# Performance work log

Measured on AMD Instinct MI355X. Metric: run time of the kernel, lower is better.

## Reference

```python
import jax, jax.numpy as jnp
import numpy as np

N, R, B, H, C, E = 4096, 8, 30, 64, 16, 131072


def setup_inputs() -> dict:
    key = jax.random.key(0)
    ks = jax.random.split(key, 11)
    s = 0.02  # small init scale for weights
    return {
        "x": jax.random.normal(ks[0], (N, N), jnp.float32),
        "edge_index": jax.random.randint(ks[1], (2, E), 0, N, jnp.int32),
        "edge_type": jax.random.randint(ks[2], (E,), 0, R, jnp.int32),
        "basis1": jax.random.normal(ks[3], (B, N, H), jnp.float32) * s,
        "att1": jax.random.normal(ks[4], (R, B), jnp.float32) * s,
        "root1": jax.random.normal(ks[5], (N, H), jnp.float32) * s,
        "bias1": jnp.zeros((H,), jnp.float32),
        "basis2": jax.random.normal(ks[6], (B, H, C), jnp.float32) * s,
        "att2": jax.random.normal(ks[7], (R, B), jnp.float32) * s,
        "root2": jax.random.normal(ks[8], (H, C), jnp.float32) * s,
        "bias2": jnp.zeros((C,), jnp.float32),
    }


def _rgcn_conv(x, src, dst, etype, deg_inv, basis, att, root, bias):
    # Basis-decomposed relation weights: W_r = sum_b att[r,b] * basis[b]
    W = jnp.einsum("rb,bio->rio", att, basis)            # [R, in, out]
    # Pre-transform every node by every relation weight (equivalent to
    # per-edge bmm(x_j, W[edge_type]) but avoids gathering [E, in] features).
    h = jnp.einsum("ni,rio->nro", x, W)                  # [N, R, out]
    msg = h[src, etype]                                  # [E, out] per-edge message
    agg = jax.ops.segment_sum(msg, dst, num_segments=N)  # scatter-add to dst
    agg = agg * deg_inv[:, None]                         # scatter-mean (aggr='mean')
    return agg + x @ root + bias                         # root/self transform + bias


def reference(x, edge_index, edge_type, basis1, att1, root1, bias1,
              basis2, att2, root2, bias2):
    src, dst = edge_index[0], edge_index[1]
    deg = jax.ops.segment_sum(jnp.ones((E,), jnp.float32), dst, num_segments=N)
    deg_inv = 1.0 / jnp.maximum(deg, 1.0)  # zero in-degree -> 0 output, as scatter_mean
    h = jax.nn.relu(_rgcn_conv(x, src, dst, edge_type, deg_inv,
                               basis1, att1, root1, bias1))
    out = _rgcn_conv(h, src, dst, edge_type, deg_inv,
                     basis2, att2, root2, bias2)
    return jax.nn.log_softmax(out, axis=1)
```

## Files before the change

kernel.cpp:

```cpp
#include <hip/hip_runtime.h>
#include <cstdint>

#define E_CNT 131072
#define N_CNT 4096

typedef short bf16x8 __attribute__((ext_vector_type(8)));
typedef float f32x4 __attribute__((ext_vector_type(4)));

__device__ __forceinline__ ushort f2bf(float f) {
  union { float f; unsigned u; } v; v.f = f;
  unsigned r = v.u + 0x7FFFu + ((v.u >> 16) & 1u);
  return (ushort)(r >> 16);
}

__global__ __launch_bounds__(256) void k_combine(const float* __restrict__ att1,
                                                 const float* __restrict__ basis1,
                                                 const float* __restrict__ root1,
                                                 ushort* __restrict__ wt1,
                                                 const int* __restrict__ dstp,
                                                 int* __restrict__ deg) {
  __shared__ float sT[32 * 33];
  int bid = blockIdx.x, t = threadIdx.x;
  if (bid < 256) {
    int i0 = (bid >> 1) * 32, o0 = (bid & 1) * 32;
    int ol = t & 31, ir = t >> 5;
    float a[8][4] = {};
    for (int b = 0; b < 30; b += 2) {
      float v0[4], v1[4];
#pragma unroll
      for (int k = 0; k < 4; ++k) {
        size_t ofs = (size_t)(i0 + ir + k * 8) * 64 + o0 + ol;
        v0[k] = basis1[(size_t)b * 262144 + ofs];
        v1[k] = basis1[(size_t)(b + 1) * 262144 + ofs];
      }
#pragma unroll
      for (int r = 0; r < 8; ++r) {
        float w0 = att1[r * 30 + b], w1 = att1[r * 30 + b + 1];
#pragma unroll
        for (int k = 0; k < 4; ++k) a[r][k] += w0 * v0[k] + w1 * v1[k];
      }
    }
    for (int r = 0; r < 8; ++r) {
#pragma unroll
      for (int k = 0; k < 4; ++k) sT[ol * 33 + ir + k * 8] = a[r][k];
      __syncthreads();
#pragma unroll
      for (int k = 0; k < 4; ++k) {
        int orow = ir + k * 8, icol = ol;
        wt1[(size_t)(r * 64 + o0 + orow) * 4096 + i0 + icol] = f2bf(sT[orow * 33 + icol]);
      }
      __syncthreads();
    }
  } else if (bid < 384) {
    int bb = bid - 256;
    int i0 = bb * 32;
    int ol = t & 31, ir = t >> 5;
    for (int oh = 0; oh < 2; ++oh) {
      int o0 = oh * 32;
#pragma unroll
      for (int k = 0; k < 4; ++k)
        sT[ol * 33 + ir + k * 8] = root1[(size_t)(i0 + ir + k * 8) * 64 + o0 + ol];
      __syncthreads();
#pragma unroll
      for (int k = 0; k < 4; ++k) {
        int orow = ir + k * 8, icol = ol;
        wt1[(size_t)(512 + o0 + orow) * 4096 + i0 + icol] = f2bf(sT[orow * 33 + icol]);
      }
      __syncthreads();
    }
  } else {
    int e = (bid - 384) * 256 + t;
    atomicAdd(&deg[dstp[e]], 1);
  }
}

__global__ __launch_bounds__(1024) void k_scan(const int* __restrict__ deg,
                                               int* __restrict__ rowptr,
                                               int* __restrict__ cursor,
                                               float* __restrict__ dinv) {
  __shared__ int part[1024];
  int t = threadIdx.x;
  int base = t * 4;
  int d0 = deg[base], d1 = deg[base + 1], d2 = deg[base + 2], d3 = deg[base + 3];
  int s = d0 + d1 + d2 + d3;
  part[t] = s;
  __syncthreads();
  for (int off = 1; off < 1024; off <<= 1) {
    int v = part[t];
    int u = (t >= off) ? part[t - off] : 0;
    __syncthreads();
    part[t] = v + u;
    __syncthreads();
  }
  int incl = part[t];
  int excl = incl - s;
  int p0 = excl, p1 = excl + d0, p2 = p1 + d1, p3 = p2 + d2;
  rowptr[base] = p0; rowptr[base + 1] = p1; rowptr[base + 2] = p2; rowptr[base + 3] = p3;
  cursor[base] = p0; cursor[base + 1] = p1; cursor[base + 2] = p2; cursor[base + 3] = p3;
  dinv[base]     = 1.0f / fmaxf((float)d0, 1.0f);
  dinv[base + 1] = 1.0f / fmaxf((float)d1, 1.0f);
  dinv[base + 2] = 1.0f / fmaxf((float)d2, 1.0f);
  dinv[base + 3] = 1.0f / fmaxf((float)d3, 1.0f);
  if (t == 1023) rowptr[4096] = incl;
}

__global__ __launch_bounds__(256) void k_mid(const int* __restrict__ srcp,
                                             const int* __restrict__ dstp,
                                             const int* __restrict__ et,
                                             int* __restrict__ cursor,
                                             int* __restrict__ spack,
                                             const float* __restrict__ att2,
                                             const float* __restrict__ basis2,
                                             const float* __restrict__ root2,
                                             float* __restrict__ w2e) {
  int bid = blockIdx.x, t = threadIdx.x;
  if (bid < 512) {
    int e = bid * 256 + t;
    int d = dstp[e];
    int pos = atomicAdd(&cursor[d], 1);
    spack[pos] = (srcp[e] << 3) | et[e];
  } else {
    int r = bid - 512;
    for (int q = t; q < 1024; q += 256) {
      float a = 0.f;
      if (r < 8) {
        for (int b = 0; b < 30; ++b) a += att2[r * 30 + b] * basis2[b * 1024 + q];
      } else {
        a = root2[q];
      }
      w2e[r * 1024 + q] = a;
    }
  }
}

__global__ __launch_bounds__(256, 5) void k_gemm1(const float* __restrict__ x,
                                                  const ushort* __restrict__ wt1,
                                                  float* __restrict__ c1) {
  __shared__ __align__(16) ushort As[128 * 64];
  __shared__ __align__(16) ushort Bs[64 * 64];
  int bid = blockIdx.x;
  int xcd = bid & 7, idx = bid >> 3;
  int bn = idx % 9, mk = idx / 9;
  int kp = xcd >> 1, bm = ((xcd & 1) << 4) + mk;
  int m0 = bm * 128, n0 = bn * 64, kbase = kp * 1024;
  int tid = threadIdx.x;
  int lane = tid & 63, wid = tid >> 6;
  int wm = wid >> 1, wn = wid & 1;

  f32x4 acc[4][2] = {};

  for (int tt = 0; tt < 16; ++tt) {
    int k0 = kbase + tt * 64;
    float4 va[4][2];
#pragma unroll
    for (int it = 0; it < 4; ++it) {
      int flat = it * 256 + tid;
      int row = flat >> 3, gg = flat & 7;
      const float* src = x + (size_t)(m0 + row) * 4096 + k0 + ((gg ^ (row & 7)) << 3);
      va[it][0] = *(const float4*)src;
      va[it][1] = *(const float4*)(src + 4);
    }
#pragma unroll
    for (int it = 0; it < 2; ++it) {
      int flat = it * 256 + tid;
      int row = flat >> 3, gg = flat & 7;
      int gcol = k0 + ((gg ^ (row & 7)) << 3);
      const ushort* g = wt1 + (size_t)(n0 + row) * 4096 + gcol;
      ushort* l = &Bs[(it * 256 + wid * 64) * 8];
      __builtin_amdgcn_global_load_lds((const __attribute__((address_space(1))) void*)g,
                                       (__attribute__((address_space(3))) void*)l, 16, 0, 0);
    }
#pragma unroll
    for (int it = 0; it < 4; ++it) {
      int flat = it * 256 + tid;
      float4 v0 = va[it][0], v1 = va[it][1];
      ushort o8[8] = {f2bf(v0.x), f2bf(v0.y), f2bf(v0.z), f2bf(v0.w),
                      f2bf(v1.x), f2bf(v1.y), f2bf(v1.z), f2bf(v1.w)};
      *(ulonglong2*)&As[flat * 8] = *(const ulonglong2*)o8;
    }
    __syncthreads();
    int q = lane >> 4, sw = lane & 7, r16 = lane & 15;
#pragma unroll
    for (int ks = 0; ks < 2; ++ks) {
      int co = ((ks * 4 + q) ^ sw) << 3;
      bf16x8 b0 = *(const bf16x8*)&Bs[(wn * 32 + 0 * 16 + r16) * 64 + co];
      bf16x8 b1 = *(const bf16x8*)&Bs[(wn * 32 + 1 * 16 + r16) * 64 + co];
      bf16x8 a0 = *(const bf16x8*)&As[(wm * 64 + 0 * 16 + r16) * 64 + co];
      bf16x8 a1 = *(const bf16x8*)&As[(wm * 64 + 1 * 16 + r16) * 64 + co];
      bf16x8 a2 = *(const bf16x8*)&As[(wm * 64 + 2 * 16 + r16) * 64 + co];
      bf16x8 a3 = *(const bf16x8*)&As[(wm * 64 + 3 * 16 + r16) * 64 + co];
      __builtin_amdgcn_s_setprio(1);
      acc[0][0] = __builtin_amdgcn_mfma_f32_16x16x32_bf16(a0, b0, acc[0][0], 0, 0, 0);
      acc[0][1] = __builtin_amdgcn_mfma_f32_16x16x32_bf16(a0, b1, acc[0][1], 0, 0, 0);
      acc[1][0] = __builtin_amdgcn_mfma_f32_16x16x32_bf16(a1, b0, acc[1][0], 0, 0, 0);
      acc[1][1] = __builtin_amdgcn_mfma_f32_16x16x32_bf16(a1, b1, acc[1][1], 0, 0, 0);
      acc[2][0] = __builtin_amdgcn_mfma_f32_16x16x32_bf16(a2, b0, acc[2][0], 0, 0, 0);
      acc[2][1] = __builtin_amdgcn_mfma_f32_16x16x32_bf16(a2, b1, acc[2][1], 0, 0, 0);
      acc[3][0] = __builtin_amdgcn_mfma_f32_16x16x32_bf16(a3, b0, acc[3][0], 0, 0, 0);
      acc[3][1] = __builtin_amdgcn_mfma_f32_16x16x32_bf16(a3, b1, acc[3][1], 0, 0, 0);
      __builtin_amdgcn_s_setprio(0);
    }
    __syncthreads();
  }

  int cf = lane & 15, rf4 = (lane >> 4) * 4;
#pragma unroll
  for (int mi = 0; mi < 4; ++mi)
#pragma unroll
    for (int ni = 0; ni < 2; ++ni) {
      int gcol = n0 + wn * 32 + ni * 16 + cf;
#pragma unroll
      for (int j = 0; j < 4; ++j) {
        int grow = m0 + wm * 64 + mi * 16 + rf4 + j;
        atomicAdd(&c1[(size_t)grow * 576 + gcol], acc[mi][ni][j]);
      }
    }
}

__global__ __launch_bounds__(256) void k_agg1h2(const float* __restrict__ c1,
                                                const int* __restrict__ rowptr,
                                                const int* __restrict__ spack,
                                                const float* __restrict__ dinv,
                                                const float* __restrict__ bias1,
                                                const float* __restrict__ w2e,
                                                float* __restrict__ h2c) {
  __shared__ float sh[4][64];
  int g = threadIdx.x >> 6, t = threadIdx.x & 63;
  int n = blockIdx.x * 4 + g;
  int s0 = rowptr[n], s1 = rowptr[n + 1];
  float acc = 0.f;
  int e = s0;
  for (; e + 3 < s1; e += 4) {
    int p0 = spack[e], p1 = spack[e + 1], p2 = spack[e + 2], p3 = spack[e + 3];
    float v0 = c1[(size_t)(p0 >> 3) * 576 + (p0 & 7) * 64 + t];
    float v1 = c1[(size_t)(p1 >> 3) * 576 + (p1 & 7) * 64 + t];
    float v2 = c1[(size_t)(p2 >> 3) * 576 + (p2 & 7) * 64 + t];
    float v3 = c1[(size_t)(p3 >> 3) * 576 + (p3 & 7) * 64 + t];
    acc += (v0 + v1) + (v2 + v3);
  }
  for (; e < s1; ++e) {
    int p = spack[e];
    acc += c1[(size_t)(p >> 3) * 576 + (p & 7) * 64 + t];
  }
  float v = acc * dinv[n] + c1[(size_t)n * 576 + 512 + t] + bias1[t];
  sh[g][t] = fmaxf(v, 0.f);
  __syncthreads();
  float* o = h2c + (size_t)n * 144;
  for (int rc = t; rc < 144; rc += 64) {
    int r9 = rc >> 4, c = rc & 15;
    const float* w = w2e + r9 * 1024 + c;
    float a = 0.f;
#pragma unroll
    for (int hh = 0; hh < 64; ++hh) a += sh[g][hh] * w[hh * 16];
    o[rc] = a;
  }
}

__global__ __launch_bounds__(64) void k_agg2(const float* __restrict__ h2c,
                                             const int* __restrict__ rowptr,
                                             const int* __restrict__ spack,
                                             const float* __restrict__ dinv,
                                             const float* __restrict__ bias2,
                                             float* __restrict__ out) {
  __shared__ float red[64];
  int n = blockIdx.x, t = threadIdx.x;
  int c = t & 15, q = t >> 4;
  int s0 = rowptr[n], s1 = rowptr[n + 1];
  float acc = 0.f;
  for (int e = s0 + q; e < s1; e += 4) {
    int p = spack[e];
    acc += h2c[(size_t)(p >> 3) * 144 + (p & 7) * 16 + c];
  }
  red[t] = acc;
  __syncthreads();
  if (t < 16) {
    float sum = red[c] + red[16 + c] + red[32 + c] + red[48 + c];
    float v = sum * dinv[n] + h2c[(size_t)n * 144 + 128 + c] + bias2[c];
    float m = v;
#pragma unroll
    for (int off = 1; off < 16; off <<= 1) m = fmaxf(m, __shfl_xor(m, off, 64));
    float ex = expf(v - m);
    float s = ex;
#pragma unroll
    for (int off = 1; off < 16; off <<= 1) s += __shfl_xor(s, off, 64);
    out[n * 16 + c] = v - m - logf(s);
  }
}

extern "C" void kernel_launch(void* const* d_in, const int* in_sizes, int n_in,
                              void* d_out, int out_size, void* d_ws, size_t ws_size,
                              hipStream_t stream) {
  const float* x      = (const float*)d_in[0];
  const int*   ei     = (const int*)d_in[1];
  const int*   et     = (const int*)d_in[2];
  const float* basis1 = (const float*)d_in[3];
  const float* att1   = (const float*)d_in[4];
  const float* root1  = (const float*)d_in[5];
  const float* bias1  = (const float*)d_in[6];
  const float* basis2 = (const float*)d_in[7];
  const float* att2   = (const float*)d_in[8];
  const float* root2  = (const float*)d_in[9];
  const float* bias2  = (const float*)d_in[10];
  float* out = (float*)d_out;

  char* ws = (char*)d_ws;
  size_t off = 0;
  auto alloc = [&](size_t bytes) {
    void* p = ws + off;
    off = (off + bytes + 255) & ~(size_t)255;
    return p;
  };
  ushort* wt1  = (ushort*)alloc((size_t)576 * 4096 * 2);
  float*  c1   = (float*)alloc((size_t)N_CNT * 576 * 4);
  float*  w2e  = (float*)alloc((size_t)9 * 64 * 16 * 4);
  float*  h2c  = (float*)alloc((size_t)N_CNT * 144 * 4);
  int*    deg    = (int*)alloc(4096 * 4);
  float*  dinv   = (float*)alloc(4096 * 4);
  int*    rowptr = (int*)alloc(4097 * 4);
  int*    cursor = (int*)alloc(4096 * 4);
  int*    spack  = (int*)alloc((size_t)E_CNT * 4);

  const int* srcp = ei;
  const int* dstp = ei + E_CNT;

  hipMemsetAsync(deg, 0, 4096 * 4, stream);
  hipMemsetAsync(c1, 0, (size_t)N_CNT * 576 * 4, stream);
  k_combine<<<896, 256, 0, stream>>>(att1, basis1, root1, wt1, dstp, deg);
  k_scan<<<1, 1024, 0, stream>>>(deg, rowptr, cursor, dinv);
  k_mid<<<521, 256, 0, stream>>>(srcp, dstp, et, cursor, spack,
                                 att2, basis2, root2, w2e);
  k_gemm1<<<1152, 256, 0, stream>>>(x, wt1, c1);
  k_agg1h2<<<1024, 256, 0, stream>>>(c1, rowptr, spack, dinv, bias1, w2e, h2c);
  k_agg2<<<4096, 64, 0, stream>>>(h2c, rowptr, spack, dinv, bias2, out);
}
```

Measured before the change: 139.7 us.

## Pre-convert x to bf16 in prep kernel and stream GEMM tiles via direct LDS loads

Adds 8192 blocks to the prep kernel that convert the fp32 x matrix to a bf16 workspace copy. The GEMM then loads A tiles with global_load_lds like the B tiles, doubles the K tile to 128, and remaps the block swizzle. This takes the fp32 load and per-thread conversion out of the GEMM inner loop and halves A-operand bytes. In exchange it adds a full extra pass over x (64MB read plus 32MB write) and doubles LDS use, which lowers occupancy.

```diff
diff --git a/kernel.cpp b/kernel.cpp
--- a/kernel.cpp
+++ b/kernel.cpp
@@ -13,12 +13,14 @@
   return (ushort)(r >> 16);
 }
 
-__global__ __launch_bounds__(256) void k_combine(const float* __restrict__ att1,
-                                                 const float* __restrict__ basis1,
-                                                 const float* __restrict__ root1,
-                                                 ushort* __restrict__ wt1,
-                                                 const int* __restrict__ dstp,
-                                                 int* __restrict__ deg) {
+__global__ __launch_bounds__(256) void k_prep(const float* __restrict__ att1,
+                                              const float* __restrict__ basis1,
+                                              const float* __restrict__ root1,
+                                              ushort* __restrict__ wt1,
+                                              const int* __restrict__ dstp,
+                                              int* __restrict__ deg,
+                                              const float4* __restrict__ x,
+                                              ushort* __restrict__ xbf) {
   __shared__ float sT[32 * 33];
   int bid = blockIdx.x, t = threadIdx.x;
   if (bid < 256) {
@@ -68,9 +70,16 @@
       }
       __syncthreads();
     }
-  } else {
+  } else if (bid < 896) {
     int e = (bid - 384) * 256 + t;
     atomicAdd(&deg[dstp[e]], 1);
+  } else {
+    int i = (bid - 896) * 256 + t;
+    float4 v0 = x[i * 2], v1 = x[i * 2 + 1];
+    ushort o[8];
+    o[0] = f2bf(v0.x); o[1] = f2bf(v0.y); o[2] = f2bf(v0.z); o[3] = f2bf(v0.w);
+    o[4] = f2bf(v1.x); o[5] = f2bf(v1.y); o[6] = f2bf(v1.z); o[7] = f2bf(v1.w);
+    *(ulonglong2*)(xbf + (size_t)i * 8) = *(const ulonglong2*)o;
   }
 }
 
@@ -133,15 +142,15 @@
   }
 }
 
-__global__ __launch_bounds__(256, 5) void k_gemm1(const float* __restrict__ x,
+__global__ __launch_bounds__(256, 3) void k_gemm1(const ushort* __restrict__ xbf,
                                                   const ushort* __restrict__ wt1,
                                                   float* __restrict__ c1) {
-  __shared__ __align__(16) ushort As[128 * 64];
-  __shared__ __align__(16) ushort Bs[64 * 64];
+  __shared__ __align__(16) ushort As[128 * 128];
+  __shared__ __align__(16) ushort Bs[64 * 128];
   int bid = blockIdx.x;
-  int xcd = bid & 7, idx = bid >> 3;
-  int bn = idx % 9, mk = idx / 9;
-  int kp = xcd >> 1, bm = ((xcd & 1) << 4) + mk;
+  int swz = (bid & 7) * 144 + (bid >> 3);
+  int kp = swz / 288, rem = swz % 288;
+  int bm = rem / 9, bn = rem % 9;
   int m0 = bm * 128, n0 = bn * 64, kbase = kp * 1024;
   int tid = threadIdx.x;
   int lane = tid & 63, wid = tid >> 6;
@@ -149,46 +158,39 @@
 
   f32x4 acc[4][2] = {};
 
-  for (int tt = 0; tt < 16; ++tt) {
-    int k0 = kbase + tt * 64;
-    float4 va[4][2];
+  for (int tt = 0; tt < 8; ++tt) {
+    int k0 = kbase + tt * 128;
+#pragma unroll
+    for (int it = 0; it < 8; ++it) {
+      int flat = it * 256 + tid;
+      int row = flat >> 4, gg = flat & 15;
+      int gcol = k0 + ((gg ^ (row & 7)) << 3);
+      const ushort* g = xbf + (size_t)(m0 + row) * 4096 + gcol;
+      ushort* l = &As[(it * 256 + wid * 64) * 8];
+      __builtin_amdgcn_global_load_lds((const __attribute__((address_space(1))) void*)g,
+                                       (__attribute__((address_space(3))) void*)l, 16, 0, 0);
+    }
 #pragma unroll
     for (int it = 0; it < 4; ++it) {
       int flat = it * 256 + tid;
-      int row = flat >> 3, gg = flat & 7;
-      const float* src = x + (size_t)(m0 + row) * 4096 + k0 + ((gg ^ (row & 7)) << 3);
-      va[it][0] = *(const float4*)src;
-      va[it][1] = *(const float4*)(src + 4);
-    }
-#pragma unroll
-    for (int it = 0; it < 2; ++it) {
-      int flat = it * 256 + tid;
-      int row = flat >> 3, gg = flat & 7;
+      int row = flat >> 4, gg = flat & 15;
       int gcol = k0 + ((gg ^ (row & 7)) << 3);
       const ushort* g = wt1 + (size_t)(n0 + row) * 4096 + gcol;
       ushort* l = &Bs[(it * 256 + wid * 64) * 8];
       __builtin_amdgcn_global_load_lds((const __attribute__((address_space(1))) void*)g,
                                        (__attribute__((address_space(3))) void*)l, 16, 0, 0);
     }
-#pragma unroll
-    for (int it = 0; it < 4; ++it) {
-      int flat = it * 256 + tid;
-      float4 v0 = va[it][0], v1 = va[it][1];
-      ushort o8[8] = {f2bf(v0.x), f2bf(v0.y), f2bf(v0.z), f2bf(v0.w),
-                      f2bf(v1.x), f2bf(v1.y), f2bf(v1.z), f2bf(v1.w)};
-      *(ulonglong2*)&As[flat * 8] = *(const ulonglong2*)o8;
-    }
     __syncthreads();
     int q = lane >> 4, sw = lane & 7, r16 = lane & 15;
 #pragma unroll
-    for (int ks = 0; ks < 2; ++ks) {
+    for (int ks = 0; ks < 4; ++ks) {
       int co = ((ks * 4 + q) ^ sw) << 3;
-      bf16x8 b0 = *(const bf16x8*)&Bs[(wn * 32 + 0 * 16 + r16) * 64 + co];
-      bf16x8 b1 = *(const bf16x8*)&Bs[(wn * 32 + 1 * 16 + r16) * 64 + co];
-      bf16x8 a0 = *(const bf16x8*)&As[(wm * 64 + 0 * 16 + r16) * 64 + co];
-      bf16x8 a1 = *(const bf16x8*)&As[(wm * 64 + 1 * 16 + r16) * 64 + co];
-      bf16x8 a2 = *(const bf16x8*)&As[(wm * 64 + 2 * 16 + r16) * 64 + co];
-      bf16x8 a3 = *(const bf16x8*)&As[(wm * 64 + 3 * 16 + r16) * 64 + co];
+      bf16x8 b0 = *(const bf16x8*)&Bs[(wn * 32 + 0 * 16 + r16) * 128 + co];
+      bf16x8 b1 = *(const bf16x8*)&Bs[(wn * 32 + 1 * 16 + r16) * 128 + co];
+      bf16x8 a0 = *(const bf16x8*)&As[(wm * 64 + 0 * 16 + r16) * 128 + co];
+      bf16x8 a1 = *(const bf16x8*)&As[(wm * 64 + 1 * 16 + r16) * 128 + co];
+      bf16x8 a2 = *(const bf16x8*)&As[(wm * 64 + 2 * 16 + r16) * 128 + co];
+      bf16x8 a3 = *(const bf16x8*)&As[(wm * 64 + 3 * 16 + r16) * 128 + co];
       __builtin_amdgcn_s_setprio(1);
       acc[0][0] = __builtin_amdgcn_mfma_f32_16x16x32_bf16(a0, b0, acc[0][0], 0, 0, 0);
       acc[0][1] = __builtin_amdgcn_mfma_f32_16x16x32_bf16(a0, b1, acc[0][1], 0, 0, 0);
@@ -310,6 +312,7 @@
     off = (off + bytes + 255) & ~(size_t)255;
     return p;
   };
+  ushort* xbf  = (ushort*)alloc((size_t)N_CNT * N_CNT * 2);
   ushort* wt1  = (ushort*)alloc((size_t)576 * 4096 * 2);
   float*  c1   = (float*)alloc((size_t)N_CNT * 576 * 4);
   float*  w2e  = (float*)alloc((size_t)9 * 64 * 16 * 4);
@@ -325,11 +328,12 @@
 
   hipMemsetAsync(deg, 0, 4096 * 4, stream);
   hipMemsetAsync(c1, 0, (size_t)N_CNT * 576 * 4, stream);
-  k_combine<<<896, 256, 0, stream>>>(att1, basis1, root1, wt1, dstp, deg);
+  k_prep<<<9088, 256, 0, stream>>>(att1, basis1, root1, wt1, dstp, deg,
+                                   (const float4*)x, xbf);
   k_scan<<<1, 1024, 0, stream>>>(deg, rowptr, cursor, dinv);
   k_mid<<<521, 256, 0, stream>>>(srcp, dstp, et, cursor, spack,
                                  att2, basis2, root2, w2e);
-  k_gemm1<<<1152, 256, 0, stream>>>(x, wt1, c1);
+  k_gemm1<<<1152, 256, 0, stream>>>(xbf, wt1, c1);
   k_agg1h2<<<1024, 256, 0, stream>>>(c1, rowptr, spack, dinv, bias1, w2e, h2c);
   k_agg2<<<4096, 64, 0, stream>>>(h2c, rowptr, spack, dinv, bias2, out);
 }
```

Result: faster. 136.2 us (-2.5%).
